# Performance work log

Measured on AMD Instinct MI355X. Metric: run time of the kernel, lower is better.

Reference implementation:

```python
import jax, jax.numpy as jnp
import numpy as np

EMBED_DIM = 1024
HEAD_DIM = 64


def setup_inputs() -> dict:
    key = jax.random.key(0)
    ks = jax.random.split(key, 7)
    s_in = EMBED_DIM ** -0.5  # torch Linear default init scale
    x = jax.random.normal(ks[0], (4, 4096, EMBED_DIM), dtype=jnp.float32)
    Wk = jax.random.uniform(ks[1], (HEAD_DIM, EMBED_DIM), jnp.float32, -s_in, s_in)
    bk = jax.random.uniform(ks[2], (HEAD_DIM,), jnp.float32, -s_in, s_in)
    Wq = jax.random.uniform(ks[3], (HEAD_DIM, EMBED_DIM), jnp.float32, -s_in, s_in)
    bq = jax.random.uniform(ks[4], (HEAD_DIM,), jnp.float32, -s_in, s_in)
    Wv = jax.random.uniform(ks[5], (HEAD_DIM, EMBED_DIM), jnp.float32, -s_in, s_in)
    bv = jax.random.uniform(ks[6], (HEAD_DIM,), jnp.float32, -s_in, s_in)
    return {"x": x, "Wq": Wq, "bq": bq, "Wk": Wk, "bk": bk, "Wv": Wv, "bv": bv}


def reference(x, Wq, bq, Wk, bk, Wv, bv):
    # torch Linear: y = x @ W.T + b
    q = jnp.einsum('btc,dc->btd', x, Wq) + bq  # [B,T,D]
    k = jnp.einsum('btc,dc->btd', x, Wk) + bk
    v = jnp.einsum('btc,dc->btd', x, Wv) + bv
    scale = HEAD_DIM ** -0.5
    # NOTE: original divides by scale (multiplies by sqrt(head_dim)) -- faithful
    scores = jnp.einsum('btd,bsd->bts', q, k) / scale  # [B,T,T]
    attn_weights = jax.nn.softmax(scores, axis=-1)
    return jnp.einsum('bts,bsd->btd', attn_weights, v)
```

## Files before the change

### kernel.cpp

```cpp
#include <hip/hip_runtime.h>

#define BATCH 4
#define SEQ   4096
#define CDIM  1024
#define DDIM  64
#define SP    72

typedef _Float16 f16;
typedef _Float16 f16x8 __attribute__((ext_vector_type(8)));
typedef _Float16 f16x4 __attribute__((ext_vector_type(4)));
typedef float    f32x4 __attribute__((ext_vector_type(4)));

#define MFMA16(a, b, c) __builtin_amdgcn_mfma_f32_16x16x32_f16((a), (b), (c), 0, 0, 0)

#define QSCALE 11.5415603f

__global__ __launch_bounds__(256) void prep_w_kernel(const float* __restrict__ Wq,
                                                     const float* __restrict__ Wk,
                                                     const float* __restrict__ Wv,
                                                     f16* __restrict__ wf) {
  int i = blockIdx.x * 256 + threadIdx.x;
  wf[i]          = (f16)Wq[i];
  wf[i + 65536]  = (f16)Wk[i];
  wf[i + 131072] = (f16)Wv[i];
}

__global__ __launch_bounds__(256) void proj_kernel(const float* __restrict__ x,
                                                   const f16* __restrict__ wf,
                                                   const float* __restrict__ bq,
                                                   const float* __restrict__ bk,
                                                   const float* __restrict__ bv,
                                                   f16* __restrict__ qs,
                                                   f16* __restrict__ ks,
                                                   f16* __restrict__ vT) {
  __shared__ __attribute__((aligned(16))) f16 lw[192][SP];
  const int tid = threadIdx.x;
  const int lane = tid & 63, w = tid >> 6;
  const int n = lane & 15, quad = lane >> 4;
  const int rowbase = blockIdx.x * 64 + w * 16;

  const int srow = tid >> 2;
  const int scol = (tid & 3) * 8;

  f32x4 acc[3][4];
#pragma unroll
  for (int m_ = 0; m_ < 3; ++m_)
#pragma unroll
    for (int t_ = 0; t_ < 4; ++t_) acc[m_][t_] = (f32x4){0.f, 0.f, 0.f, 0.f};

  const float* xrow = x + (size_t)(rowbase + n) * CDIM + quad * 8;

  f16x8 wreg[3];
  f32x4 xr0, xr1;
#define WLOAD(KC)                                                                    \
  {                                                                                  \
    _Pragma("unroll") for (int i = 0; i < 3; ++i)                                    \
        wreg[i] = *(const f16x8*)(wf + (size_t)(i * 64 + srow) * CDIM + (KC) + scol); \
  }
#define XLOAD(KC)                        \
  {                                      \
    xr0 = *(const f32x4*)(xrow + (KC));  \
    xr1 = *(const f32x4*)(xrow + (KC) + 4); \
  }

  WLOAD(0);
  XLOAD(0);
  for (int kc = 0; kc < CDIM; kc += 32) {
#pragma unroll
    for (int i = 0; i < 3; ++i) *(f16x8*)&lw[i * 64 + srow][scol] = wreg[i];
    __syncthreads();
    if (kc + 32 < CDIM) WLOAD(kc + 32);
    f16x8 a;
#pragma unroll
    for (int j = 0; j < 4; ++j) { a[j] = (f16)xr0[j]; a[4 + j] = (f16)xr1[j]; }
    if (kc + 32 < CDIM) XLOAD(kc + 32);
#pragma unroll
    for (int mat = 0; mat < 3; ++mat)
#pragma unroll
      for (int tile = 0; tile < 4; ++tile) {
        const f16x8 bf = *(const f16x8*)&lw[mat * 64 + tile * 16 + n][quad * 8];
        acc[mat][tile] = MFMA16(a, bf, acc[mat][tile]);
      }
    __syncthreads();
  }

  const float* bias_p[3] = {bq, bk, bv};
#pragma unroll
  for (int mat = 0; mat < 3; ++mat)
#pragma unroll
    for (int tile = 0; tile < 4; ++tile) {
      const int d = tile * 16 + n;
      const float bias = bias_p[mat][d];
      const int row0 = rowbase + quad * 4;
      f32x4 a = acc[mat][tile];
      if (mat == 0) {
#pragma unroll
        for (int r = 0; r < 4; ++r)
          qs[(size_t)(row0 + r) * DDIM + d] = (f16)((a[r] + bias) * QSCALE);
      } else if (mat == 1) {
#pragma unroll
        for (int r = 0; r < 4; ++r)
          ks[(size_t)(row0 + r) * DDIM + d] = (f16)(a[r] + bias);
      } else {
        const int bb = row0 >> 12;
        const int t = row0 & (SEQ - 1);
        f16x4 pk;
#pragma unroll
        for (int r = 0; r < 4; ++r) pk[r] = (f16)(a[r] + bias);
        *(f16x4*)(vT + (size_t)(bb * 64 + d) * SEQ + t) = pk;
      }
    }
}

template <bool SPLIT2>
__global__ __launch_bounds__(256) void attn_kernel(const f16* __restrict__ qs,
                                                   const f16* __restrict__ ks,
                                                   const f16* __restrict__ vT,
                                                   float* __restrict__ outp,
                                                   float* __restrict__ pm,
                                                   float* __restrict__ pl) {
  __shared__ __attribute__((aligned(16))) f16 lk[64][SP];
  __shared__ __attribute__((aligned(16))) f16 lv[64][SP];
  __shared__ __attribute__((aligned(16))) f16 pb[4][16][SP];

  const int tid = threadIdx.x;
  const int lane = tid & 63, w = tid >> 6;
  const int n = lane & 15, quad = lane >> 4;

  const int rowblk = SPLIT2 ? (blockIdx.x >> 1) : blockIdx.x;
  const int split  = SPLIT2 ? (blockIdx.x & 1) : 0;
  const int kbase  = split * (SEQ / 2);
  const int NC     = SPLIT2 ? (SEQ / 2 / 64) : (SEQ / 64);

  const int row0 = rowblk * 64 + w * 16;
  const int bb = row0 >> 12;

  const f16* qrow = qs + (size_t)(row0 + n) * DDIM + quad * 8;
  const f16x8 qlo = *(const f16x8*)qrow;
  const f16x8 qhi = *(const f16x8*)(qrow + 32);

  const f16* kb = ks + (size_t)bb * SEQ * DDIM;
  const f16* vb = vT + (size_t)bb * DDIM * SEQ;

  const int srow = tid >> 3;
  const int scol = (tid & 7) * 8;

  f16x8 kr0, kr1, vr0, vr1;
#define LOADC(T0)                                                        \
  {                                                                      \
    kr0 = *(const f16x8*)(kb + (size_t)((T0) + srow) * DDIM + scol);     \
    kr1 = *(const f16x8*)(kb + (size_t)((T0) + srow + 32) * DDIM + scol);\
    vr0 = *(const f16x8*)(vb + (size_t)srow * SEQ + (T0) + scol);        \
    vr1 = *(const f16x8*)(vb + (size_t)(srow + 32) * SEQ + (T0) + scol); \
  }

  f32x4 acc[4];
  float mrow[4], llane[4];
#pragma unroll
  for (int r = 0; r < 4; ++r) { mrow[r] = -1e30f; llane[r] = 0.f; }
#pragma unroll
  for (int t_ = 0; t_ < 4; ++t_) acc[t_] = (f32x4){0.f, 0.f, 0.f, 0.f};

  LOADC(kbase);
  for (int c = 0; c < NC; ++c) {
    *(f16x8*)&lk[srow][scol] = kr0;
    *(f16x8*)&lk[srow + 32][scol] = kr1;
    *(f16x8*)&lv[srow][scol] = vr0;
    *(f16x8*)&lv[srow + 32][scol] = vr1;
    __syncthreads();
    if (c + 1 < NC) LOADC(kbase + (c + 1) * 64);

    f32x4 s[4];
#pragma unroll
    for (int st = 0; st < 4; ++st) {
      const f16x8 klo = *(const f16x8*)&lk[st * 16 + n][quad * 8];
      const f16x8 khi = *(const f16x8*)&lk[st * 16 + n][32 + quad * 8];
      f32x4 z = (f32x4){0.f, 0.f, 0.f, 0.f};
      z = MFMA16(qlo, klo, z);
      s[st] = MFMA16(qhi, khi, z);
    }

    float alpha[4];
#pragma unroll
    for (int r = 0; r < 4; ++r) {
      float mloc = fmaxf(fmaxf(s[0][r], s[1][r]), fmaxf(s[2][r], s[3][r]));
      mloc = fmaxf(mloc, __shfl_xor(mloc, 1));
      mloc = fmaxf(mloc, __shfl_xor(mloc, 2));
      mloc = fmaxf(mloc, __shfl_xor(mloc, 4));
      mloc = fmaxf(mloc, __shfl_xor(mloc, 8));
      const float mnew = fmaxf(mrow[r], mloc);
      alpha[r] = __builtin_amdgcn_exp2f(mrow[r] - mnew);
      mrow[r] = mnew;
      const float p0 = __builtin_amdgcn_exp2f(s[0][r] - mnew);
      const float p1 = __builtin_amdgcn_exp2f(s[1][r] - mnew);
      const float p2 = __builtin_amdgcn_exp2f(s[2][r] - mnew);
      const float p3 = __builtin_amdgcn_exp2f(s[3][r] - mnew);
      llane[r] = llane[r] * alpha[r] + ((p0 + p1) + (p2 + p3));
      const int prow = quad * 4 + r;
      pb[w][prow][n] = (f16)p0;
      pb[w][prow][16 + n] = (f16)p1;
      pb[w][prow][32 + n] = (f16)p2;
      pb[w][prow][48 + n] = (f16)p3;
    }
#pragma unroll
    for (int tile = 0; tile < 4; ++tile) {
      acc[tile][0] *= alpha[0];
      acc[tile][1] *= alpha[1];
      acc[tile][2] *= alpha[2];
      acc[tile][3] *= alpha[3];
    }
    __builtin_amdgcn_wave_barrier();
    const f16x8 pa0 = *(const f16x8*)&pb[w][n][quad * 8];
    const f16x8 pa1 = *(const f16x8*)&pb[w][n][32 + quad * 8];
#pragma unroll
    for (int tile = 0; tile < 4; ++tile) {
      const f16x8 vlo = *(const f16x8*)&lv[tile * 16 + n][quad * 8];
      const f16x8 vhi = *(const f16x8*)&lv[tile * 16 + n][32 + quad * 8];
      acc[tile] = MFMA16(pa0, vlo, acc[tile]);
      acc[tile] = MFMA16(pa1, vhi, acc[tile]);
    }
    __syncthreads();
  }

  float lred[4];
#pragma unroll
  for (int r = 0; r < 4; ++r) {
    float l = llane[r];
    l += __shfl_xor(l, 1);
    l += __shfl_xor(l, 2);
    l += __shfl_xor(l, 4);
    l += __shfl_xor(l, 8);
    lred[r] = l;
  }

  if (SPLIT2) {
    float* pacc = outp;
#pragma unroll
    for (int r = 0; r < 4; ++r) {
      const int grow = row0 + quad * 4 + r;
#pragma unroll
      for (int tile = 0; tile < 4; ++tile)
        pacc[((size_t)split * BATCH * SEQ + grow) * DDIM + tile * 16 + n] = acc[tile][r];
      if (n == 0) {
        pm[split * BATCH * SEQ + grow] = mrow[r];
        pl[split * BATCH * SEQ + grow] = lred[r];
      }
    }
  } else {
#pragma unroll
    for (int r = 0; r < 4; ++r) {
      const float inv = 1.0f / lred[r];
      const int grow = row0 + quad * 4 + r;
#pragma unroll
      for (int tile = 0; tile < 4; ++tile)
        outp[(size_t)grow * DDIM + tile * 16 + n] = acc[tile][r] * inv;
    }
  }
}

__global__ __launch_bounds__(256) void combine_kernel(const float* __restrict__ pacc,
                                                      const float* __restrict__ pm,
                                                      const float* __restrict__ pl,
                                                      float* __restrict__ out) {
  const int idx = blockIdx.x * 256 + threadIdx.x;
  const int row = idx >> 4;
  const int c = (idx & 15) * 4;
  const float m0 = pm[row], m1 = pm[BATCH * SEQ + row];
  const float l0 = pl[row], l1 = pl[BATCH * SEQ + row];
  const float mm = fmaxf(m0, m1);
  const float e0 = __builtin_amdgcn_exp2f(m0 - mm);
  const float e1 = __builtin_amdgcn_exp2f(m1 - mm);
  const float inv = 1.0f / (l0 * e0 + l1 * e1);
  const f32x4 a0 = *(const f32x4*)(pacc + (size_t)row * DDIM + c);
  const f32x4 a1 = *(const f32x4*)(pacc + (size_t)(BATCH * SEQ + row) * DDIM + c);
  f32x4 o;
#pragma unroll
  for (int j = 0; j < 4; ++j) o[j] = (a0[j] * e0 + a1[j] * e1) * inv;
  *(f32x4*)(out + (size_t)row * DDIM + c) = o;
}

extern "C" void kernel_launch(void* const* d_in, const int* in_sizes, int n_in,
                              void* d_out, int out_size, void* d_ws, size_t ws_size,
                              hipStream_t stream) {
  const float* x  = (const float*)d_in[0];
  const float* Wq = (const float*)d_in[1];
  const float* bq = (const float*)d_in[2];
  const float* Wk = (const float*)d_in[3];
  const float* bk = (const float*)d_in[4];
  const float* Wv = (const float*)d_in[5];
  const float* bv = (const float*)d_in[6];
  float* out = (float*)d_out;

  f16* wf = (f16*)d_ws;
  f16* qs = wf + 3 * 65536;
  f16* ks = qs + (size_t)BATCH * SEQ * DDIM;
  f16* vT = ks + (size_t)BATCH * SEQ * DDIM;
  char* endf16 = (char*)(vT + (size_t)BATCH * SEQ * DDIM);

  float* pacc = (float*)endf16;
  float* pm   = pacc + (size_t)2 * BATCH * SEQ * DDIM;
  float* pl   = pm + (size_t)2 * BATCH * SEQ;
  const size_t need = (size_t)((char*)(pl + (size_t)2 * BATCH * SEQ) - (char*)d_ws);
  const bool split2 = ws_size >= need;

  prep_w_kernel<<<dim3(256), dim3(256), 0, stream>>>(Wq, Wk, Wv, wf);
  proj_kernel<<<dim3(256), dim3(256), 0, stream>>>(x, wf, bq, bk, bv, qs, ks, vT);
  if (split2) {
    attn_kernel<true><<<dim3(512), dim3(256), 0, stream>>>(qs, ks, vT, pacc, pm, pl);
    combine_kernel<<<dim3(BATCH * SEQ * 16 / 256), dim3(256), 0, stream>>>(pacc, pm, pl, out);
  } else {
    attn_kernel<false><<<dim3(256), dim3(256), 0, stream>>>(qs, ks, vT, out, nullptr, nullptr);
  }
}
```

Measured before the change: 186.6 us.

## Restructure attention to register-fed K/V with 32 rows per wave and 4-way split

The attention kernel drops the LDS staging of K and V. Each wave now loads its K and V fragments straight from global memory into registers, double-buffering the K fragments across chunks, and handles 32 query rows instead of 16. It also swaps the MFMA operand order so the softmax reductions become cross-quad shuffles, and splits the key range four ways with a generalized combine kernel. The weight-prep kernel is folded into the projection through in-register packed fp16 conversion. The risks are heavier global and L2 traffic, since K and V are no longer shared across the waves of a block, and higher register pressure under launch_bounds(256,2).

```diff
diff --git a/kernel.cpp b/kernel.cpp
--- a/kernel.cpp
+++ b/kernel.cpp
@@ -4,29 +4,43 @@
 #define SEQ   4096
 #define CDIM  1024
 #define DDIM  64
+#define NROW  (BATCH * SEQ)
 #define SP    72
+#define SPB   72
 
 typedef _Float16 f16;
 typedef _Float16 f16x8 __attribute__((ext_vector_type(8)));
 typedef _Float16 f16x4 __attribute__((ext_vector_type(4)));
+typedef __fp16   h16x2 __attribute__((ext_vector_type(2)));
 typedef float    f32x4 __attribute__((ext_vector_type(4)));
 
 #define MFMA16(a, b, c) __builtin_amdgcn_mfma_f32_16x16x32_f16((a), (b), (c), 0, 0, 0)
 
 #define QSCALE 11.5415603f
 
-__global__ __launch_bounds__(256) void prep_w_kernel(const float* __restrict__ Wq,
-                                                     const float* __restrict__ Wk,
-                                                     const float* __restrict__ Wv,
-                                                     f16* __restrict__ wf) {
-  int i = blockIdx.x * 256 + threadIdx.x;
-  wf[i]          = (f16)Wq[i];
-  wf[i + 65536]  = (f16)Wk[i];
-  wf[i + 131072] = (f16)Wv[i];
+__device__ inline f16x8 cvt8(f32x4 a, f32x4 b) {
+  h16x2 p0 = __builtin_amdgcn_cvt_pkrtz(a[0], a[1]);
+  h16x2 p1 = __builtin_amdgcn_cvt_pkrtz(a[2], a[3]);
+  h16x2 p2 = __builtin_amdgcn_cvt_pkrtz(b[0], b[1]);
+  h16x2 p3 = __builtin_amdgcn_cvt_pkrtz(b[2], b[3]);
+  f16x8 r;
+  r[0] = p0[0]; r[1] = p0[1]; r[2] = p1[0]; r[3] = p1[1];
+  r[4] = p2[0]; r[5] = p2[1]; r[6] = p3[0]; r[7] = p3[1];
+  return r;
+}
+
+__device__ inline f16x4 cvt4(float a, float b, float c, float d) {
+  h16x2 lo = __builtin_amdgcn_cvt_pkrtz(a, b);
+  h16x2 hi = __builtin_amdgcn_cvt_pkrtz(c, d);
+  f16x4 r;
+  r[0] = lo[0]; r[1] = lo[1]; r[2] = hi[0]; r[3] = hi[1];
+  return r;
 }
 
 __global__ __launch_bounds__(256) void proj_kernel(const float* __restrict__ x,
-                                                   const f16* __restrict__ wf,
+                                                   const float* __restrict__ Wq,
+                                                   const float* __restrict__ Wk,
+                                                   const float* __restrict__ Wv,
                                                    const float* __restrict__ bq,
                                                    const float* __restrict__ bk,
                                                    const float* __restrict__ bv,
@@ -38,10 +52,11 @@
   const int lane = tid & 63, w = tid >> 6;
   const int n = lane & 15, quad = lane >> 4;
   const int rowbase = blockIdx.x * 64 + w * 16;
-
   const int srow = tid >> 2;
   const int scol = (tid & 3) * 8;
 
+  const float* Wm[3] = {Wq, Wk, Wv};
+
   f32x4 acc[3][4];
 #pragma unroll
   for (int m_ = 0; m_ < 3; ++m_)
@@ -50,16 +65,19 @@
 
   const float* xrow = x + (size_t)(rowbase + n) * CDIM + quad * 8;
 
-  f16x8 wreg[3];
+  f32x4 wr[3][2];
   f32x4 xr0, xr1;
-#define WLOAD(KC)                                                                    \
-  {                                                                                  \
-    _Pragma("unroll") for (int i = 0; i < 3; ++i)                                    \
-        wreg[i] = *(const f16x8*)(wf + (size_t)(i * 64 + srow) * CDIM + (KC) + scol); \
-  }
-#define XLOAD(KC)                        \
-  {                                      \
-    xr0 = *(const f32x4*)(xrow + (KC));  \
+#define WLOAD(KC)                                                          \
+  {                                                                        \
+    _Pragma("unroll") for (int i = 0; i < 3; ++i) {                        \
+      const float* p = Wm[i] + (size_t)srow * CDIM + (KC) + scol;          \
+      wr[i][0] = *(const f32x4*)p;                                         \
+      wr[i][1] = *(const f32x4*)(p + 4);                                   \
+    }                                                                      \
+  }
+#define XLOAD(KC)                          \
+  {                                        \
+    xr0 = *(const f32x4*)(xrow + (KC));    \
     xr1 = *(const f32x4*)(xrow + (KC) + 4); \
   }
 
@@ -67,12 +85,10 @@
   XLOAD(0);
   for (int kc = 0; kc < CDIM; kc += 32) {
 #pragma unroll
-    for (int i = 0; i < 3; ++i) *(f16x8*)&lw[i * 64 + srow][scol] = wreg[i];
+    for (int i = 0; i < 3; ++i) *(f16x8*)&lw[i * 64 + srow][scol] = cvt8(wr[i][0], wr[i][1]);
     __syncthreads();
     if (kc + 32 < CDIM) WLOAD(kc + 32);
-    f16x8 a;
-#pragma unroll
-    for (int j = 0; j < 4; ++j) { a[j] = (f16)xr0[j]; a[4 + j] = (f16)xr1[j]; }
+    const f16x8 a = cvt8(xr0, xr1);
     if (kc + 32 < CDIM) XLOAD(kc + 32);
 #pragma unroll
     for (int mat = 0; mat < 3; ++mat)
@@ -104,160 +120,161 @@
       } else {
         const int bb = row0 >> 12;
         const int t = row0 & (SEQ - 1);
-        f16x4 pk;
-#pragma unroll
-        for (int r = 0; r < 4; ++r) pk[r] = (f16)(a[r] + bias);
+        f16x4 pk = cvt4(a[0] + bias, a[1] + bias, a[2] + bias, a[3] + bias);
         *(f16x4*)(vT + (size_t)(bb * 64 + d) * SEQ + t) = pk;
       }
     }
 }
 
-template <bool SPLIT2>
-__global__ __launch_bounds__(256) void attn_kernel(const f16* __restrict__ qs,
-                                                   const f16* __restrict__ ks,
-                                                   const f16* __restrict__ vT,
-                                                   float* __restrict__ outp,
-                                                   float* __restrict__ pm,
-                                                   float* __restrict__ pl) {
-  __shared__ __attribute__((aligned(16))) f16 lk[64][SP];
-  __shared__ __attribute__((aligned(16))) f16 lv[64][SP];
-  __shared__ __attribute__((aligned(16))) f16 pb[4][16][SP];
-
-  const int tid = threadIdx.x;
-  const int lane = tid & 63, w = tid >> 6;
+template <int NSPLIT>
+__global__ __launch_bounds__(256, 2) void attn_kernel(const f16* __restrict__ qs,
+                                                      const f16* __restrict__ ks,
+                                                      const f16* __restrict__ vT,
+                                                      float* __restrict__ outp,
+                                                      float* __restrict__ pm,
+                                                      float* __restrict__ pl) {
+  __shared__ __attribute__((aligned(16))) f16 pb[4][32][SPB];
+  const int tid = threadIdx.x, lane = tid & 63, w = tid >> 6;
   const int n = lane & 15, quad = lane >> 4;
-
-  const int rowblk = SPLIT2 ? (blockIdx.x >> 1) : blockIdx.x;
-  const int split  = SPLIT2 ? (blockIdx.x & 1) : 0;
-  const int kbase  = split * (SEQ / 2);
-  const int NC     = SPLIT2 ? (SEQ / 2 / 64) : (SEQ / 64);
-
-  const int row0 = rowblk * 64 + w * 16;
+  const int split = blockIdx.x & (NSPLIT - 1);
+  const int rowgrp = (blockIdx.x / NSPLIT) * 4 + w;
+  const int row0 = rowgrp * 32;
   const int bb = row0 >> 12;
-
-  const f16* qrow = qs + (size_t)(row0 + n) * DDIM + quad * 8;
-  const f16x8 qlo = *(const f16x8*)qrow;
-  const f16x8 qhi = *(const f16x8*)(qrow + 32);
+  const int kbase = split * (SEQ / NSPLIT);
+  const int NC = SEQ / NSPLIT / 64;
 
   const f16* kb = ks + (size_t)bb * SEQ * DDIM;
   const f16* vb = vT + (size_t)bb * DDIM * SEQ;
 
-  const int srow = tid >> 3;
-  const int scol = (tid & 7) * 8;
-
-  f16x8 kr0, kr1, vr0, vr1;
-#define LOADC(T0)                                                        \
-  {                                                                      \
-    kr0 = *(const f16x8*)(kb + (size_t)((T0) + srow) * DDIM + scol);     \
-    kr1 = *(const f16x8*)(kb + (size_t)((T0) + srow + 32) * DDIM + scol);\
-    vr0 = *(const f16x8*)(vb + (size_t)srow * SEQ + (T0) + scol);        \
-    vr1 = *(const f16x8*)(vb + (size_t)(srow + 32) * SEQ + (T0) + scol); \
-  }
-
-  f32x4 acc[4];
-  float mrow[4], llane[4];
-#pragma unroll
-  for (int r = 0; r < 4; ++r) { mrow[r] = -1e30f; llane[r] = 0.f; }
-#pragma unroll
-  for (int t_ = 0; t_ < 4; ++t_) acc[t_] = (f32x4){0.f, 0.f, 0.f, 0.f};
-
-  LOADC(kbase);
-  for (int c = 0; c < NC; ++c) {
-    *(f16x8*)&lk[srow][scol] = kr0;
-    *(f16x8*)&lk[srow + 32][scol] = kr1;
-    *(f16x8*)&lv[srow][scol] = vr0;
-    *(f16x8*)&lv[srow + 32][scol] = vr1;
-    __syncthreads();
-    if (c + 1 < NC) LOADC(kbase + (c + 1) * 64);
-
-    f32x4 s[4];
-#pragma unroll
-    for (int st = 0; st < 4; ++st) {
-      const f16x8 klo = *(const f16x8*)&lk[st * 16 + n][quad * 8];
-      const f16x8 khi = *(const f16x8*)&lk[st * 16 + n][32 + quad * 8];
-      f32x4 z = (f32x4){0.f, 0.f, 0.f, 0.f};
-      z = MFMA16(qlo, klo, z);
-      s[st] = MFMA16(qhi, khi, z);
-    }
-
-    float alpha[4];
-#pragma unroll
-    for (int r = 0; r < 4; ++r) {
-      float mloc = fmaxf(fmaxf(s[0][r], s[1][r]), fmaxf(s[2][r], s[3][r]));
-      mloc = fmaxf(mloc, __shfl_xor(mloc, 1));
-      mloc = fmaxf(mloc, __shfl_xor(mloc, 2));
-      mloc = fmaxf(mloc, __shfl_xor(mloc, 4));
-      mloc = fmaxf(mloc, __shfl_xor(mloc, 8));
-      const float mnew = fmaxf(mrow[r], mloc);
-      alpha[r] = __builtin_amdgcn_exp2f(mrow[r] - mnew);
-      mrow[r] = mnew;
-      const float p0 = __builtin_amdgcn_exp2f(s[0][r] - mnew);
-      const float p1 = __builtin_amdgcn_exp2f(s[1][r] - mnew);
-      const float p2 = __builtin_amdgcn_exp2f(s[2][r] - mnew);
-      const float p3 = __builtin_amdgcn_exp2f(s[3][r] - mnew);
-      llane[r] = llane[r] * alpha[r] + ((p0 + p1) + (p2 + p3));
-      const int prow = quad * 4 + r;
-      pb[w][prow][n] = (f16)p0;
-      pb[w][prow][16 + n] = (f16)p1;
-      pb[w][prow][32 + n] = (f16)p2;
-      pb[w][prow][48 + n] = (f16)p3;
-    }
-#pragma unroll
-    for (int tile = 0; tile < 4; ++tile) {
-      acc[tile][0] *= alpha[0];
-      acc[tile][1] *= alpha[1];
-      acc[tile][2] *= alpha[2];
-      acc[tile][3] *= alpha[3];
-    }
+  f16x8 qf[2][2];
+#pragma unroll
+  for (int g = 0; g < 2; ++g)
+#pragma unroll
+    for (int h = 0; h < 2; ++h)
+      qf[g][h] = *(const f16x8*)(qs + (size_t)(row0 + g * 16 + n) * DDIM + h * 32 + quad * 8);
+
+  f32x4 acc[2][4];
+  float m[2] = {-1e30f, -1e30f}, ll[2] = {0.f, 0.f};
+#pragma unroll
+  for (int g = 0; g < 2; ++g)
+#pragma unroll
+    for (int t = 0; t < 4; ++t) acc[g][t] = (f32x4){0.f, 0.f, 0.f, 0.f};
+
+  f16x8 kfA[4][2], kfB[4][2], vf[4][2];
+
+  auto kload = [&](f16x8(&DST)[4][2], int kb0) {
+#pragma unroll
+    for (int st = 0; st < 4; ++st)
+#pragma unroll
+      for (int h = 0; h < 2; ++h)
+        DST[st][h] = *(const f16x8*)(kb + (size_t)(kb0 + st * 16 + n) * DDIM + h * 32 + quad * 8);
+  };
+  auto vload = [&](int kb0) {
+#pragma unroll
+    for (int t = 0; t < 4; ++t)
+#pragma unroll
+      for (int kk = 0; kk < 2; ++kk)
+        vf[t][kk] = *(const f16x8*)(vb + (size_t)(t * 16 + n) * SEQ + kb0 + kk * 32 + quad * 8);
+  };
+
+  auto chunk = [&](f16x8(&KF)[4][2], f16x8(&KN)[4][2], int c) {
+    const int kb0 = kbase + c * 64;
+    vload(kb0);
+    f32x4 s[2][4];
+#pragma unroll
+    for (int g = 0; g < 2; ++g)
+#pragma unroll
+      for (int st = 0; st < 4; ++st) {
+        f32x4 z = (f32x4){0.f, 0.f, 0.f, 0.f};
+        z = MFMA16(KF[st][0], qf[g][0], z);
+        s[g][st] = MFMA16(KF[st][1], qf[g][1], z);
+      }
+    const int cn = (c + 1 < NC) ? (c + 1) : (NC - 1);
+    kload(KN, kbase + cn * 64);
+
     __builtin_amdgcn_wave_barrier();
-    const f16x8 pa0 = *(const f16x8*)&pb[w][n][quad * 8];
-    const f16x8 pa1 = *(const f16x8*)&pb[w][n][32 + quad * 8];
-#pragma unroll
-    for (int tile = 0; tile < 4; ++tile) {
-      const f16x8 vlo = *(const f16x8*)&lv[tile * 16 + n][quad * 8];
-      const f16x8 vhi = *(const f16x8*)&lv[tile * 16 + n][32 + quad * 8];
-      acc[tile] = MFMA16(pa0, vlo, acc[tile]);
-      acc[tile] = MFMA16(pa1, vhi, acc[tile]);
-    }
-    __syncthreads();
-  }
-
-  float lred[4];
-#pragma unroll
-  for (int r = 0; r < 4; ++r) {
-    float l = llane[r];
-    l += __shfl_xor(l, 1);
-    l += __shfl_xor(l, 2);
-    l += __shfl_xor(l, 4);
-    l += __shfl_xor(l, 8);
-    lred[r] = l;
-  }
-
-  if (SPLIT2) {
-    float* pacc = outp;
-#pragma unroll
-    for (int r = 0; r < 4; ++r) {
-      const int grow = row0 + quad * 4 + r;
-#pragma unroll
-      for (int tile = 0; tile < 4; ++tile)
-        pacc[((size_t)split * BATCH * SEQ + grow) * DDIM + tile * 16 + n] = acc[tile][r];
-      if (n == 0) {
-        pm[split * BATCH * SEQ + grow] = mrow[r];
-        pl[split * BATCH * SEQ + grow] = lred[r];
+#pragma unroll
+    for (int g = 0; g < 2; ++g) {
+      f32x4 mx;
+#pragma unroll
+      for (int r = 0; r < 4; ++r)
+        mx[r] = fmaxf(fmaxf(s[g][0][r], s[g][1][r]), fmaxf(s[g][2][r], s[g][3][r]));
+      float mloc = fmaxf(fmaxf(mx[0], mx[1]), fmaxf(mx[2], mx[3]));
+      mloc = fmaxf(mloc, __shfl_xor(mloc, 16));
+      mloc = fmaxf(mloc, __shfl_xor(mloc, 32));
+      const float mnew = fmaxf(m[g], mloc);
+      const float alpha = __builtin_amdgcn_exp2f(m[g] - mnew);
+      m[g] = mnew;
+      float psum = 0.f;
+#pragma unroll
+      for (int st = 0; st < 4; ++st) {
+        f32x4 p;
+#pragma unroll
+        for (int r = 0; r < 4; ++r) p[r] = __builtin_amdgcn_exp2f(s[g][st][r] - mnew);
+        psum += (p[0] + p[1]) + (p[2] + p[3]);
+        *(f16x4*)&pb[w][g * 16 + n][st * 16 + quad * 4] = cvt4(p[0], p[1], p[2], p[3]);
+      }
+      ll[g] = ll[g] * alpha + psum;
+#pragma unroll
+      for (int t = 0; t < 4; ++t) acc[g][t] *= alpha;
+    }
+    __builtin_amdgcn_wave_barrier();
+#pragma unroll
+    for (int g = 0; g < 2; ++g) {
+      const f16x8 pa0 = *(const f16x8*)&pb[w][g * 16 + n][quad * 8];
+      const f16x8 pa1 = *(const f16x8*)&pb[w][g * 16 + n][32 + quad * 8];
+#pragma unroll
+      for (int t = 0; t < 4; ++t) {
+        acc[g][t] = MFMA16(vf[t][0], pa0, acc[g][t]);
+        acc[g][t] = MFMA16(vf[t][1], pa1, acc[g][t]);
+      }
+    }
+  };
+
+  kload(kfA, kbase);
+  for (int c = 0; c < NC; c += 2) {
+    chunk(kfA, kfB, c);
+    chunk(kfB, kfA, c + 1);
+  }
+
+  float lred[2];
+#pragma unroll
+  for (int g = 0; g < 2; ++g) {
+    float l = ll[g];
+    l += __shfl_xor(l, 16);
+    l += __shfl_xor(l, 32);
+    lred[g] = l;
+  }
+
+  if (NSPLIT == 1) {
+#pragma unroll
+    for (int g = 0; g < 2; ++g) {
+      const float inv = 1.0f / lred[g];
+      const int q = row0 + g * 16 + n;
+#pragma unroll
+      for (int t = 0; t < 4; ++t) {
+        f32x4 o = acc[g][t];
+#pragma unroll
+        for (int r = 0; r < 4; ++r) o[r] *= inv;
+        *(f32x4*)(outp + (size_t)q * DDIM + t * 16 + quad * 4) = o;
       }
     }
   } else {
 #pragma unroll
-    for (int r = 0; r < 4; ++r) {
-      const float inv = 1.0f / lred[r];
-      const int grow = row0 + quad * 4 + r;
-#pragma unroll
-      for (int tile = 0; tile < 4; ++tile)
-        outp[(size_t)grow * DDIM + tile * 16 + n] = acc[tile][r] * inv;
-    }
-  }
-}
-
+    for (int g = 0; g < 2; ++g) {
+      const int q = row0 + g * 16 + n;
+#pragma unroll
+      for (int t = 0; t < 4; ++t)
+        *(f32x4*)(outp + ((size_t)split * NROW + q) * DDIM + t * 16 + quad * 4) = acc[g][t];
+      if (quad == 0) {
+        pm[split * NROW + q] = m[g];
+        pl[split * NROW + q] = lred[g];
+      }
+    }
+  }
+}
+
+template <int NSPLIT>
 __global__ __launch_bounds__(256) void combine_kernel(const float* __restrict__ pacc,
                                                       const float* __restrict__ pm,
                                                       const float* __restrict__ pl,
@@ -265,17 +282,22 @@
   const int idx = blockIdx.x * 256 + threadIdx.x;
   const int row = idx >> 4;
   const int c = (idx & 15) * 4;
-  const float m0 = pm[row], m1 = pm[BATCH * SEQ + row];
-  const float l0 = pl[row], l1 = pl[BATCH * SEQ + row];
-  const float mm = fmaxf(m0, m1);
-  const float e0 = __builtin_amdgcn_exp2f(m0 - mm);
-  const float e1 = __builtin_amdgcn_exp2f(m1 - mm);
-  const float inv = 1.0f / (l0 * e0 + l1 * e1);
-  const f32x4 a0 = *(const f32x4*)(pacc + (size_t)row * DDIM + c);
-  const f32x4 a1 = *(const f32x4*)(pacc + (size_t)(BATCH * SEQ + row) * DDIM + c);
-  f32x4 o;
-#pragma unroll
-  for (int j = 0; j < 4; ++j) o[j] = (a0[j] * e0 + a1[j] * e1) * inv;
+  float mm = pm[row];
+#pragma unroll
+  for (int s = 1; s < NSPLIT; ++s) mm = fmaxf(mm, pm[s * NROW + row]);
+  float L = 0.f;
+  f32x4 o = (f32x4){0.f, 0.f, 0.f, 0.f};
+#pragma unroll
+  for (int s = 0; s < NSPLIT; ++s) {
+    const float e = __builtin_amdgcn_exp2f(pm[s * NROW + row] - mm);
+    L += pl[s * NROW + row] * e;
+    const f32x4 a = *(const f32x4*)(pacc + ((size_t)s * NROW + row) * DDIM + c);
+#pragma unroll
+    for (int j = 0; j < 4; ++j) o[j] += a[j] * e;
+  }
+  const float inv = 1.0f / L;
+#pragma unroll
+  for (int j = 0; j < 4; ++j) o[j] *= inv;
   *(f32x4*)(out + (size_t)row * DDIM + c) = o;
 }
 
@@ -291,24 +313,29 @@
   const float* bv = (const float*)d_in[6];
   float* out = (float*)d_out;
 
-  f16* wf = (f16*)d_ws;
-  f16* qs = wf + 3 * 65536;
-  f16* ks = qs + (size_t)BATCH * SEQ * DDIM;
-  f16* vT = ks + (size_t)BATCH * SEQ * DDIM;
-  char* endf16 = (char*)(vT + (size_t)BATCH * SEQ * DDIM);
+  f16* qs = (f16*)d_ws;
+  f16* ks = qs + (size_t)NROW * DDIM;
+  f16* vT = ks + (size_t)NROW * DDIM;
+  char* endf16 = (char*)(vT + (size_t)NROW * DDIM);
 
   float* pacc = (float*)endf16;
-  float* pm   = pacc + (size_t)2 * BATCH * SEQ * DDIM;
-  float* pl   = pm + (size_t)2 * BATCH * SEQ;
-  const size_t need = (size_t)((char*)(pl + (size_t)2 * BATCH * SEQ) - (char*)d_ws);
-  const bool split2 = ws_size >= need;
-
-  prep_w_kernel<<<dim3(256), dim3(256), 0, stream>>>(Wq, Wk, Wv, wf);
-  proj_kernel<<<dim3(256), dim3(256), 0, stream>>>(x, wf, bq, bk, bv, qs, ks, vT);
-  if (split2) {
-    attn_kernel<true><<<dim3(512), dim3(256), 0, stream>>>(qs, ks, vT, pacc, pm, pl);
-    combine_kernel<<<dim3(BATCH * SEQ * 16 / 256), dim3(256), 0, stream>>>(pacc, pm, pl, out);
+  const size_t base = (size_t)(endf16 - (char*)d_ws);
+  const size_t need4 = base + (size_t)4 * NROW * (DDIM + 2) * 4;
+  const size_t need2 = base + (size_t)2 * NROW * (DDIM + 2) * 4;
+
+  proj_kernel<<<dim3(256), dim3(256), 0, stream>>>(x, Wq, Wk, Wv, bq, bk, bv, qs, ks, vT);
+
+  if (ws_size >= need4) {
+    float* pm = pacc + (size_t)4 * NROW * DDIM;
+    float* pl = pm + (size_t)4 * NROW;
+    attn_kernel<4><<<dim3(128 * 4), dim3(256), 0, stream>>>(qs, ks, vT, pacc, pm, pl);
+    combine_kernel<4><<<dim3(NROW * 16 / 256), dim3(256), 0, stream>>>(pacc, pm, pl, out);
+  } else if (ws_size >= need2) {
+    float* pm = pacc + (size_t)2 * NROW * DDIM;
+    float* pl = pm + (size_t)2 * NROW;
+    attn_kernel<2><<<dim3(128 * 2), dim3(256), 0, stream>>>(qs, ks, vT, pacc, pm, pl);
+    combine_kernel<2><<<dim3(NROW * 16 / 256), dim3(256), 0, stream>>>(pacc, pm, pl, out);
   } else {
-    attn_kernel<false><<<dim3(256), dim3(256), 0, stream>>>(qs, ks, vT, out, nullptr, nullptr);
-  }
-}
+    attn_kernel<1><<<dim3(128), dim3(256), 0, stream>>>(qs, ks, vT, out, nullptr, nullptr);
+  }
+}
```

Measured after the change: 190.7 us. +2.2%, slower.
